# Kernel tuning notes

Measured on AMD Instinct MI355X. Metric: run time of the kernel, lower is better.

Reference implementation:

```python
import math
import jax, jax.numpy as jnp
import numpy as np

C = 1024
H = 16
HD = C // H
T = 2048
B = 2
EPS = 1e-5


def setup_inputs() -> dict:
    key = jax.random.key(0)
    ks = jax.random.split(key, 8)
    s = 0.02
    return {
        "x": jax.random.normal(ks[0], (B, T, C), dtype=jnp.float32),
        "ln1_g": jnp.ones((C,), jnp.float32),
        "ln1_b": jnp.zeros((C,), jnp.float32),
        "w_attn": jax.random.normal(ks[1], (C, 3 * C), dtype=jnp.float32) * s,
        "b_attn": jnp.zeros((3 * C,), jnp.float32),
        "w_proj": jax.random.normal(ks[2], (C, C), dtype=jnp.float32) * s,
        "b_proj": jnp.zeros((C,), jnp.float32),
        "ln2_g": jnp.ones((C,), jnp.float32),
        "ln2_b": jnp.zeros((C,), jnp.float32),
        "w_fc": jax.random.normal(ks[3], (C, 4 * C), dtype=jnp.float32) * s,
        "b_fc": jnp.zeros((4 * C,), jnp.float32),
        "w_fc2": jax.random.normal(ks[4], (4 * C, C), dtype=jnp.float32) * s,
        "b_fc2": jnp.zeros((C,), jnp.float32),
    }


def _layernorm(x, g, b):
    mu = jnp.mean(x, axis=-1, keepdims=True)
    var = jnp.mean((x - mu) ** 2, axis=-1, keepdims=True)
    return (x - mu) * jax.lax.rsqrt(var + EPS) * g + b


def _attention(x, w_attn, b_attn, w_proj, b_proj):
    Bb, Tt, Cc = x.shape
    qkv = x @ w_attn + b_attn  # (B,T,3C)
    q, k, v = jnp.split(qkv, 3, axis=-1)
    # (B,H,T,HD)
    q = q.reshape(Bb, Tt, H, HD).transpose(0, 2, 1, 3)
    k = k.reshape(Bb, Tt, H, HD).transpose(0, 2, 1, 3)
    v = v.reshape(Bb, Tt, H, HD).transpose(0, 2, 1, 3)
    scale = 1.0 / math.sqrt(HD)
    attn = jnp.einsum("bhqd,bhkd->bhqk", q, k) * scale
    causal = jnp.tril(jnp.ones((Tt, Tt), dtype=bool))
    attn = jnp.where(causal[None, None], attn, -jnp.inf)
    attn = jax.nn.softmax(attn, axis=-1)
    out = jnp.einsum("bhqk,bhkd->bhqd", attn, v)
    out = out.transpose(0, 2, 1, 3).reshape(Bb, Tt, Cc)
    return out @ w_proj + b_proj


def _mlp(x, w_fc, b_fc, w_fc2, b_fc2):
    h = jax.nn.gelu(x @ w_fc + b_fc, approximate=True)
    return h @ w_fc2 + b_fc2


def reference(x, ln1_g, ln1_b, w_attn, b_attn, w_proj, b_proj,
              ln2_g, ln2_b, w_fc, b_fc, w_fc2, b_fc2):
    x = x + _attention(_layernorm(x, ln1_g, ln1_b), w_attn, b_attn, w_proj, b_proj)
    x = x + _mlp(_layernorm(x, ln2_g, ln2_b), w_fc, b_fc, w_fc2, b_fc2)
    return x
```

## Files before the change

### kernel.cpp

```cpp
#include <hip/hip_runtime.h>
#include <math.h>

#define TB 2
#define TT 2048
#define TC 1024
#define TH 16
#define THD 64
#define TM (TB*TT)
#define NQT 32

typedef __bf16 bf16x8 __attribute__((ext_vector_type(8)));
typedef float f32x4 __attribute__((ext_vector_type(4)));
typedef unsigned short u16x8 __attribute__((ext_vector_type(8)));
typedef unsigned short u16x4 __attribute__((ext_vector_type(4)));

__device__ __forceinline__ unsigned short f2bf(float f){
    unsigned int u = __builtin_bit_cast(unsigned int, f);
    u = (u + 0x7FFFu + ((u >> 16) & 1u)) >> 16;
    return (unsigned short)u;
}
__device__ __forceinline__ float bf2f(unsigned short h){
    unsigned int u = ((unsigned int)h) << 16;
    return __builtin_bit_cast(float, u);
}
__device__ __forceinline__ bf16x8 ldbf8(const unsigned short* p){
    return __builtin_bit_cast(bf16x8, *(const u16x8*)p);
}
__device__ __forceinline__ void gl_lds16(const void* g, void* l){
    __builtin_amdgcn_global_load_lds(
        (const __attribute__((address_space(1))) unsigned int*)g,
        (__attribute__((address_space(3))) unsigned int*)l,
        16, 0, 0);
}
__device__ __forceinline__ float gelu_tanh(float v){
    float u = 2.0f * 0.7978845608028654f * (v + 0.044715f * v * v * v);
    u = fminf(fmaxf(u, -30.f), 30.f);
    float e = __expf(u);
    return 0.5f * v * (1.f + (e - 1.f) / (e + 1.f));
}

__global__ __launch_bounds__(256)
void convert_all(const float* __restrict__ w_attn, const float* __restrict__ w_proj,
                 const float* __restrict__ w_fc,   const float* __restrict__ w_fc2,
                 unsigned short* __restrict__ wattnT, unsigned short* __restrict__ wprojT,
                 unsigned short* __restrict__ wfcT,   unsigned short* __restrict__ wfc2T){
    __shared__ float tile[32][33];
    const int bid = blockIdx.x;
    const float* in; unsigned short* out; int K, N, bx, by;
    if (bid < 3072)      { in=w_attn; out=wattnT; K=1024; N=3072; bx=bid%96;  by=bid/96; }
    else if (bid < 4096) { int lo=bid-3072; in=w_proj; out=wprojT; K=1024; N=1024; bx=lo%32;  by=lo/32; }
    else if (bid < 8192) { int lo=bid-4096; in=w_fc;   out=wfcT;   K=1024; N=4096; bx=lo%128; by=lo/128; }
    else                 { int lo=bid-8192; in=w_fc2;  out=wfc2T;  K=4096; N=1024; bx=lo%32;  by=lo/32; }
    int tx = threadIdx.x, ty = threadIdx.y;
    int n0 = bx * 32, k0 = by * 32;
    #pragma unroll
    for (int i = 0; i < 4; i++)
        tile[ty + 8*i][tx] = in[(size_t)(k0 + ty + 8*i) * N + n0 + tx];
    __syncthreads();
    #pragma unroll
    for (int i = 0; i < 4; i++)
        out[(size_t)(n0 + ty + 8*i) * K + k0 + tx] = f2bf(tile[tx][ty + 8*i]);
}

__global__ __launch_bounds__(256)
void ln_kernel(const float* __restrict__ x, const float* __restrict__ g,
               const float* __restrict__ be, unsigned short* __restrict__ y){
    const int row = blockIdx.x, t = threadIdx.x;
    const float4* xr = (const float4*)(x + (size_t)row * TC);
    float4 v = xr[t];
    float s  = v.x + v.y + v.z + v.w;
    float s2 = v.x*v.x + v.y*v.y + v.z*v.z + v.w*v.w;
    #pragma unroll
    for (int off = 32; off; off >>= 1){
        s  += __shfl_down(s,  off);
        s2 += __shfl_down(s2, off);
    }
    __shared__ float red[8];
    int l = t & 63, wv = t >> 6;
    if (l == 0){ red[wv] = s; red[4 + wv] = s2; }
    __syncthreads();
    float S  = red[0] + red[1] + red[2] + red[3];
    float S2 = red[4] + red[5] + red[6] + red[7];
    float mu = S * (1.f / TC);
    float var = S2 * (1.f / TC) - mu * mu;
    float rs = rsqrtf(var + 1e-5f);
    int c = t * 4;
    float4 gg = *(const float4*)(g + c);
    float4 bb = *(const float4*)(be + c);
    u16x4 o;
    o[0] = f2bf((v.x - mu) * rs * gg.x + bb.x);
    o[1] = f2bf((v.y - mu) * rs * gg.y + bb.y);
    o[2] = f2bf((v.z - mu) * rs * gg.z + bb.z);
    o[3] = f2bf((v.w - mu) * rs * gg.w + bb.w);
    *(u16x4*)(y + (size_t)row * TC + c) = o;
}

template<int EPI>
__global__ __launch_bounds__(256, 2)
void gemm_bt(const unsigned short* __restrict__ A,
             const unsigned short* __restrict__ Bt,
             const float* __restrict__ bias,
             const float* __restrict__ resid,
             void* __restrict__ outv,
             int M, int N, int K){
    __shared__ unsigned short lA[128 * 32];
    __shared__ unsigned short lB[128 * 32];
    const int t = threadIdx.x, w = t >> 6, l = t & 63, lr = l & 15, lg = l >> 4;
    const int nt = N >> 7;
    const int nwg = gridDim.x;
    const int bid = blockIdx.x;
    int wg = (nwg & 7) ? bid : ((bid & 7) * (nwg >> 3) + (bid >> 3));
    const int bm = wg / nt, bn = wg % nt;
    const int row0 = bm << 7, col0 = bn << 7;
    const int wr = w >> 1, wc = w & 1;

    f32x4 acc[4][4];
    #pragma unroll
    for (int i = 0; i < 4; i++)
        #pragma unroll
        for (int j = 0; j < 4; j++) acc[i][j] = (f32x4){0.f,0.f,0.f,0.f};

    const char* Ag = (const char*)(A + (size_t)(row0 + (t >> 2)) * K) + (t & 3) * 16;
    const char* Bg = (const char*)(Bt + (size_t)(col0 + (t >> 2)) * K) + (t & 3) * 16;
    const size_t rstep = (size_t)64 * K * 2;
    char* lAw = (char*)lA + w * 1024;
    char* lBw = (char*)lB + w * 1024;

    for (int k0 = 0; k0 < K; k0 += 32){
        size_t kb = (size_t)k0 * 2;
        gl_lds16(Ag + kb,          lAw);
        gl_lds16(Ag + kb + rstep,  lAw + 4096);
        gl_lds16(Bg + kb,          lBw);
        gl_lds16(Bg + kb + rstep,  lBw + 4096);
        __syncthreads();
        bf16x8 af[4], bfr[4];
        #pragma unroll
        for (int mi = 0; mi < 4; mi++)
            af[mi] = ldbf8(lA + (wr*64 + mi*16 + lr) * 32 + lg * 8);
        #pragma unroll
        for (int ni = 0; ni < 4; ni++)
            bfr[ni] = ldbf8(lB + (wc*64 + ni*16 + lr) * 32 + lg * 8);
        #pragma unroll
        for (int mi = 0; mi < 4; mi++)
            #pragma unroll
            for (int ni = 0; ni < 4; ni++)
                acc[mi][ni] = __builtin_amdgcn_mfma_f32_16x16x32_bf16(
                    af[mi], bfr[ni], acc[mi][ni], 0, 0, 0);
        __syncthreads();
    }

    float bcol[4];
    #pragma unroll
    for (int ni = 0; ni < 4; ni++) bcol[ni] = bias[col0 + wc*64 + ni*16 + lr];
    #pragma unroll
    for (int mi = 0; mi < 4; mi++){
        #pragma unroll
        for (int j = 0; j < 4; j++){
            int row = row0 + wr*64 + mi*16 + lg*4 + j;
            size_t base = (size_t)row * N + col0 + wc*64 + lr;
            #pragma unroll
            for (int ni = 0; ni < 4; ni++){
                float v = acc[mi][ni][j] + bcol[ni];
                size_t idx = base + (size_t)ni * 16;
                if (EPI == 0)      ((unsigned short*)outv)[idx] = f2bf(v);
                else if (EPI == 1) ((float*)outv)[idx] = v + resid[idx];
                else               ((unsigned short*)outv)[idx] = f2bf(gelu_tanh(v));
            }
        }
    }
}

template<int MH>
__device__ __forceinline__ void gloadA(const unsigned short* bufA, bf16x8 (&af)[4][2],
                                       int wm, int lr, int sl0, int sl1){
    #pragma unroll
    for (int i = 0; i < 4; i++){
        int lrow = (wm*128 + (MH*4 + i)*16 + lr) * 64;
        af[i][0] = ldbf8(bufA + lrow + sl0);
        af[i][1] = ldbf8(bufA + lrow + sl1);
    }
}
__device__ __forceinline__ void gloadB(const unsigned short* bufB, bf16x8 (&bfr)[4][2],
                                       int wn, int lr, int sl0, int sl1){
    #pragma unroll
    for (int i = 0; i < 4; i++){
        int brow = (wn*64 + i*16 + lr) * 64;
        bfr[i][0] = ldbf8(bufB + brow + sl0);
        bfr[i][1] = ldbf8(bufB + brow + sl1);
    }
}
template<int MH, int NH>
__device__ __forceinline__ void gmma(const bf16x8 (&af)[4][2], const bf16x8 (&bfr)[4][2],
                                     f32x4 (&acc)[8][4]){
    #pragma unroll
    for (int i = 0; i < 4; i++)
        #pragma unroll
        for (int j = 0; j < 2; j++){
            f32x4& a = acc[MH*4 + i][NH*2 + j];
            a = __builtin_amdgcn_mfma_f32_16x16x32_bf16(af[i][0], bfr[NH*2+j][0], a, 0,0,0);
            a = __builtin_amdgcn_mfma_f32_16x16x32_bf16(af[i][1], bfr[NH*2+j][1], a, 0,0,0);
        }
}

#define G256_LOOP(NT_, KBEG_)                                                   \
    for (int tk = 0; tk < (NT_); ++tk){                                         \
        const int cur = tk & 1;                                                 \
        const bool more = (tk + 1) < (NT_);                                     \
        const unsigned short* bufA = &lds[cur][0][0];                           \
        const unsigned short* bufB = &lds[cur][1][0];                           \
        if (more){                                                              \
            stage(cur ^ 1, (KBEG_) + (tk + 1)*64, 0);                           \
            asm volatile("s_waitcnt vmcnt(2)" ::: "memory");                    \
        } else {                                                                \
            asm volatile("s_waitcnt vmcnt(0)" ::: "memory");                    \
        }                                                                       \
        __builtin_amdgcn_s_barrier();                                           \
        bf16x8 af[4][2], bfr[4][2];                                             \
        gloadA<0>(bufA, af, wm, lr, sl0, sl1);                                  \
        gloadB(bufB, bfr, wn, lr, sl0, sl1);                                    \
        if (more) stage(cur ^ 1, (KBEG_) + (tk + 1)*64, 1);                     \
        __builtin_amdgcn_s_barrier();                                           \
        asm volatile("s_waitcnt lgkmcnt(0)" ::: "memory");                      \
        __builtin_amdgcn_sched_barrier(0);                                      \
        __builtin_amdgcn_s_setprio(1);                                          \
        gmma<0,0>(af, bfr, acc);                                                \
        __builtin_amdgcn_s_setprio(0);                                          \
        __builtin_amdgcn_s_barrier();                                           \
        if (more) stage(cur ^ 1, (KBEG_) + (tk + 1)*64, 2);                     \
        __builtin_amdgcn_s_setprio(1);                                          \
        gmma<0,1>(af, bfr, acc);                                                \
        __builtin_amdgcn_s_setprio(0);                                          \
        __builtin_amdgcn_s_barrier();                                           \
        gloadA<1>(bufA, af, wm, lr, sl0, sl1);                                  \
        if (more) stage(cur ^ 1, (KBEG_) + (tk + 1)*64, 3);                     \
        __builtin_amdgcn_s_barrier();                                           \
        asm volatile("s_waitcnt lgkmcnt(0)" ::: "memory");                      \
        __builtin_amdgcn_sched_barrier(0);                                      \
        __builtin_amdgcn_s_setprio(1);                                          \
        gmma<1,0>(af, bfr, acc);                                                \
        __builtin_amdgcn_s_setprio(0);                                          \
        __builtin_amdgcn_s_barrier();                                           \
        __builtin_amdgcn_s_setprio(1);                                          \
        gmma<1,1>(af, bfr, acc);                                                \
        __builtin_amdgcn_s_setprio(0);                                          \
        __builtin_amdgcn_s_barrier();                                           \
    }

template<int EPI>
__global__ __launch_bounds__(512, 1)
void gemm256(const unsigned short* __restrict__ A,
             const unsigned short* __restrict__ Bt,
             const float* __restrict__ bias,
             void* __restrict__ outv,
             int M, int N, int K){
    __shared__ unsigned short lds[2][2][256*64];
    const int t = threadIdx.x;
    const int w = t >> 6, l = t & 63, lr = l & 15, lg = l >> 4;
    const int wm = w >> 2, wn = w & 3;
    const int lr7 = lr & 7;
    const int sl0 = (lg ^ lr7) << 3;
    const int sl1 = ((4 + lg) ^ lr7) << 3;
    const int nbn = N >> 8;
    const int nwg = (M >> 8) * nbn;
    const int bid = blockIdx.x;
    const int wg = (nwg & 7) ? bid : ((bid & 7) * (nwg >> 3) + (bid >> 3));
    const int bm = wg / nbn, bn = wg % nbn;
    const size_t row0 = (size_t)bm << 8, col0 = (size_t)bn << 8;
    const int NT = K >> 6;

    f32x4 acc[8][4];
    #pragma unroll
    for (int i = 0; i < 8; i++)
        #pragma unroll
        for (int j = 0; j < 4; j++) acc[i][j] = (f32x4){0.f,0.f,0.f,0.f};

    int rowc[4], slogc[4];
    #pragma unroll
    for (int c = 0; c < 4; c++){
        int seg = t + (c << 9);
        rowc[c]  = seg >> 3;
        slogc[c] = (((seg & 7) ^ ((seg >> 3) & 7)) << 3);
    }
    const unsigned short* Abase = A  + row0 * K;
    const unsigned short* Bbase = Bt + col0 * K;
    auto stage = [&](int buf, int kofs, int c){
        int seg = t + (c << 9);
        const unsigned short* sa = Abase + (size_t)rowc[c] * K + kofs + slogc[c];
        const unsigned short* sb = Bbase + (size_t)rowc[c] * K + kofs + slogc[c];
        gl_lds16(sa, (void*)&lds[buf][0][seg * 8]);
        gl_lds16(sb, (void*)&lds[buf][1][seg * 8]);
    };

    #pragma unroll
    for (int c = 0; c < 4; c++) stage(0, 0, c);

    G256_LOOP(NT, 0)

    float bcol[4];
    #pragma unroll
    for (int ni = 0; ni < 4; ni++) bcol[ni] = bias[col0 + wn*64 + ni*16 + lr];
    unsigned short* outp = (unsigned short*)outv;
    #pragma unroll
    for (int mi = 0; mi < 8; mi++){
        #pragma unroll
        for (int j = 0; j < 4; j++){
            size_t row = row0 + wm*128 + mi*16 + lg*4 + j;
            size_t base = row * N + col0 + wn*64 + lr;
            #pragma unroll
            for (int ni = 0; ni < 4; ni++){
                float v = acc[mi][ni][j] + bcol[ni];
                size_t idx = base + (size_t)ni * 16;
                if (EPI == 0) outp[idx] = f2bf(v);
                else          outp[idx] = f2bf(gelu_tanh(v));
            }
        }
    }
}

__global__ __launch_bounds__(512, 1)
void gemm256sk(const unsigned short* __restrict__ A,
               const unsigned short* __restrict__ Bt,
               unsigned short* __restrict__ pout,
               int M, int N, int K, int klen){
    __shared__ unsigned short lds[2][2][256*64];
    const int t = threadIdx.x;
    const int w = t >> 6, l = t & 63, lr = l & 15, lg = l >> 4;
    const int wm = w >> 2, wn = w & 3;
    const int lr7 = lr & 7;
    const int sl0 = (lg ^ lr7) << 3;
    const int sl1 = ((4 + lg) ^ lr7) << 3;
    const int nbn = N >> 8;
    const int ntile = (M >> 8) * nbn;
    const int nwg = gridDim.x;
    const int bid = blockIdx.x;
    int wg = (nwg & 7) ? bid : ((bid & 7) * (nwg >> 3) + (bid >> 3));
    const int kh = wg / ntile;
    wg -= kh * ntile;
    const int bm = wg / nbn, bn = wg % nbn;
    const size_t row0 = (size_t)bm << 8, col0 = (size_t)bn << 8;
    const int NT = klen >> 6;
    const int kbeg = kh * klen;

    f32x4 acc[8][4];
    #pragma unroll
    for (int i = 0; i < 8; i++)
        #pragma unroll
        for (int j = 0; j < 4; j++) acc[i][j] = (f32x4){0.f,0.f,0.f,0.f};

    int rowc[4], slogc[4];
    #pragma unroll
    for (int c = 0; c < 4; c++){
        int seg = t + (c << 9);
        rowc[c]  = seg >> 3;
        slogc[c] = (((seg & 7) ^ ((seg >> 3) & 7)) << 3);
    }
    const unsigned short* Abase = A  + row0 * K;
    const unsigned short* Bbase = Bt + col0 * K;
    auto stage = [&](int buf, int kofs, int c){
        int seg = t + (c << 9);
        const unsigned short* sa = Abase + (size_t)rowc[c] * K + kofs + slogc[c];
        const unsigned short* sb = Bbase + (size_t)rowc[c] * K + kofs + slogc[c];
        gl_lds16(sa, (void*)&lds[buf][0][seg * 8]);
        gl_lds16(sb, (void*)&lds[buf][1][seg * 8]);
    };

    #pragma unroll
    for (int c = 0; c < 4; c++) stage(0, kbeg, c);

    G256_LOOP(NT, kbeg)

    unsigned short* outp = pout + (size_t)kh * M * N;
    #pragma unroll
    for (int mi = 0; mi < 8; mi++){
        #pragma unroll
        for (int j = 0; j < 4; j++){
            size_t row = row0 + wm*128 + mi*16 + lg*4 + j;
            size_t base = row * N + col0 + wn*64 + lr;
            #pragma unroll
            for (int ni = 0; ni < 4; ni++)
                outp[base + (size_t)ni * 16] = f2bf(acc[mi][ni][j]);
        }
    }
}

__global__ __launch_bounds__(256)
void combine_k4(const unsigned short* __restrict__ p,
                const float* __restrict__ bias, const float* __restrict__ resid,
                float* __restrict__ out){
    const size_t PS = (size_t)TM * TC;
    const int total = TM * TC / 4;
    for (int i = blockIdx.x * 256 + threadIdx.x; i < total; i += gridDim.x * 256){
        int e = i * 4;
        u16x4 a0 = *(const u16x4*)(p + e);
        u16x4 a1 = *(const u16x4*)(p + PS + e);
        u16x4 a2 = *(const u16x4*)(p + 2*PS + e);
        u16x4 a3 = *(const u16x4*)(p + 3*PS + e);
        float4 r = *(const float4*)(resid + e);
        float4 bb = *(const float4*)(bias + (e & (TC - 1)));
        float4 o;
        o.x = bf2f(a0[0]) + bf2f(a1[0]) + bf2f(a2[0]) + bf2f(a3[0]) + r.x + bb.x;
        o.y = bf2f(a0[1]) + bf2f(a1[1]) + bf2f(a2[1]) + bf2f(a3[1]) + r.y + bb.y;
        o.z = bf2f(a0[2]) + bf2f(a1[2]) + bf2f(a2[2]) + bf2f(a3[2]) + r.z + bb.z;
        o.w = bf2f(a0[3]) + bf2f(a1[3]) + bf2f(a2[3]) + bf2f(a3[3]) + r.w + bb.w;
        *(float4*)(out + e) = o;
    }
}

__global__ __launch_bounds__(256)
void vtrans(const unsigned short* __restrict__ qkv, unsigned short* __restrict__ vTg){
    __shared__ unsigned short lt[64][68];
    int kt = blockIdx.x & (NQT - 1);
    int bh = blockIdx.x >> 5;
    int h = bh & (TH - 1), b = bh >> 4;
    int t = threadIdx.x;
    int r = t >> 2, c4 = t & 3;
    const unsigned short* src = qkv + (size_t)(b*TT + kt*64 + r) * (3*TC) + 2*TC + h*THD;
    u16x8 a0 = *(const u16x8*)(src + c4*8);
    u16x8 a1 = *(const u16x8*)(src + 32 + c4*8);
    #pragma unroll
    for (int j = 0; j < 8; j++){
        lt[r][c4*8 + j]      = a0[j];
        lt[r][32 + c4*8 + j] = a1[j];
    }
    __syncthreads();
    int d = t >> 2;
    unsigned short* dst = vTg + ((size_t)bh * NQT + kt) * (64*80) + (size_t)d * 80;
    u16x8 o0, o1;
    #pragma unroll
    for (int j = 0; j < 8; j++){
        o0[j] = lt[c4*8 + j][d];
        o1[j] = lt[32 + c4*8 + j][d];
    }
    *(u16x8*)(dst + c4*8)      = o0;
    *(u16x8*)(dst + 32 + c4*8) = o1;
}

__global__ __launch_bounds__(256, 3)
void attn_kernel(const unsigned short* __restrict__ qkv,
                 const unsigned short* __restrict__ vTg,
                 unsigned short* __restrict__ attn_out){
    __shared__ unsigned short kbuf[2][64*64];
    __shared__ unsigned short vbuf[2][64*64];
    __shared__ unsigned short pl[4][16*72];

    const int bid = blockIdx.x;
    const int qrank = bid >> 5;
    const int bh = bid & 31;
    const int h = bh & (TH - 1), b = bh >> 4;
    const int qb = 31 - qrank;
    const int q0 = qb << 6;
    const int t = threadIdx.x, w = t >> 6, l = t & 63, lr = l & 15, lg = l >> 4;
    const int lr7 = lr & 7;
    const int sl0 = (lg ^ lr7) << 3;
    const int sl1 = ((4 + lg) ^ lr7) << 3;
    const float SC = 0.18033688011112042f;

    const int NKT = qb + 1;
    const int qrow_base = q0 + w*16;

    const int vt0 = t, vt1 = t + 256;
    const int sr0 = vt0 >> 3, sr1 = vt1 >> 3;
    const int sc0 = ((vt0 & 7) ^ (sr0 & 7)) * 8;
    const int sc1 = ((vt1 & 7) ^ (sr1 & 7)) * 8;
    const unsigned short* kg0 = qkv + (size_t)(b*TT + sr0) * (3*TC) + TC + h*THD + sc0;
    const unsigned short* kg1 = qkv + (size_t)(b*TT + sr1) * (3*TC) + TC + h*THD + sc1;
    const unsigned short* vg0 = vTg + (size_t)bh * (NQT*64*80) + (size_t)sr0 * 80 + sc0;
    const unsigned short* vg1 = vTg + (size_t)bh * (NQT*64*80) + (size_t)sr1 * 80 + sc1;
    const size_t kstep = (size_t)64 * (3*TC);

    auto stage = [&](int kt, int buf){
        gl_lds16(kg0 + (size_t)kt*kstep,   (void*)&kbuf[buf][vt0*8]);
        gl_lds16(kg1 + (size_t)kt*kstep,   (void*)&kbuf[buf][vt1*8]);
        gl_lds16(vg0 + (size_t)kt*(64*80), (void*)&vbuf[buf][vt0*8]);
        gl_lds16(vg1 + (size_t)kt*(64*80), (void*)&vbuf[buf][vt1*8]);
    };

    const unsigned short* qr =
        qkv + (size_t)(b*TT + qrow_base + lr) * (3*TC) + h*THD;
    bf16x8 q0f = ldbf8(qr + lg*8), q1f = ldbf8(qr + 32 + lg*8);

    bf16x8 ones;
    #pragma unroll
    for (int i = 0; i < 8; i++) ones[i] = (__bf16)1.0f;

    f32x4 o[5];
    float m[4];
    #pragma unroll
    for (int i = 0; i < 5; i++) o[i] = (f32x4){0.f,0.f,0.f,0.f};
    #pragma unroll
    for (int i = 0; i < 4; i++) m[i] = -1e30f;

    unsigned short* plw = &pl[w][0];

    stage(0, 0);
    for (int kt = 0; kt < NKT; ++kt){
        const int cur = kt & 1;
        const bool more = (kt + 1) < NKT;
        if (more){
            stage(kt + 1, cur ^ 1);
            asm volatile("s_waitcnt vmcnt(4)" ::: "memory");
        } else {
            asm volatile("s_waitcnt vmcnt(0)" ::: "memory");
        }
        __builtin_amdgcn_s_barrier();

        const unsigned short* kb = &kbuf[cur][0];
        f32x4 s[4];
        __builtin_amdgcn_s_setprio(1);
        #pragma unroll
        for (int cb = 0; cb < 4; cb++){
            bf16x8 ka = ldbf8(kb + (cb*16 + lr)*64 + sl0);
            bf16x8 kbf = ldbf8(kb + (cb*16 + lr)*64 + sl1);
            f32x4 z = (f32x4){0.f,0.f,0.f,0.f};
            z = __builtin_amdgcn_mfma_f32_16x16x32_bf16(q0f, ka, z, 0,0,0);
            z = __builtin_amdgcn_mfma_f32_16x16x32_bf16(q1f, kbf, z, 0,0,0);
            s[cb] = z;
        }
        __builtin_amdgcn_s_setprio(0);
        if (kt == qb){
            #pragma unroll
            for (int cb = 0; cb < 4; cb++)
                #pragma unroll
                for (int j = 0; j < 4; j++)
                    if (kt*64 + cb*16 + lr > qrow_base + lg*4 + j) s[cb][j] = -1e30f;
        }
        float mloc[4];
        #pragma unroll
        for (int j = 0; j < 4; j++)
            mloc[j] = fmaxf(fmaxf(s[0][j], s[1][j]), fmaxf(s[2][j], s[3][j]));
        #pragma unroll
        for (int off = 1; off < 16; off <<= 1)
            #pragma unroll
            for (int j = 0; j < 4; j++)
                mloc[j] = fmaxf(mloc[j], __shfl_xor(mloc[j], off));
        bool grow = (mloc[0]*SC > m[0]) || (mloc[1]*SC > m[1]) ||
                    (mloc[2]*SC > m[2]) || (mloc[3]*SC > m[3]);
        if (__any(grow)){
            float al[4];
            #pragma unroll
            for (int j = 0; j < 4; j++){
                float mn = fmaxf(m[j], mloc[j] * SC);
                al[j] = exp2f(m[j] - mn);
                m[j] = mn;
            }
            #pragma unroll
            for (int db = 0; db < 5; db++)
                #pragma unroll
                for (int j = 0; j < 4; j++) o[db][j] *= al[j];
        }
        #pragma unroll
        for (int cb = 0; cb < 4; cb++)
            #pragma unroll
            for (int j = 0; j < 4; j++){
                float e = exp2f(__builtin_fmaf(s[cb][j], SC, -m[j]));
                ((__bf16*)plw)[(lg*4 + j)*72 + cb*16 + lr] = (__bf16)e;
            }
        const unsigned short* vb = &vbuf[cur][0];
        bf16x8 pa0 = ldbf8(plw + lr*72 + lg*8);
        bf16x8 pa1 = ldbf8(plw + lr*72 + 32 + lg*8);
        __builtin_amdgcn_s_setprio(1);
        #pragma unroll
        for (int db = 0; db < 4; db++){
            bf16x8 va = ldbf8(vb + (db*16 + lr)*64 + sl0);
            bf16x8 vbf = ldbf8(vb + (db*16 + lr)*64 + sl1);
            o[db] = __builtin_amdgcn_mfma_f32_16x16x32_bf16(pa0, va, o[db], 0,0,0);
            o[db] = __builtin_amdgcn_mfma_f32_16x16x32_bf16(pa1, vbf, o[db], 0,0,0);
        }
        o[4] = __builtin_amdgcn_mfma_f32_16x16x32_bf16(pa0, ones, o[4], 0,0,0);
        o[4] = __builtin_amdgcn_mfma_f32_16x16x32_bf16(pa1, ones, o[4], 0,0,0);
        __builtin_amdgcn_s_setprio(0);

        __builtin_amdgcn_s_barrier();
    }

    __bf16* aout = (__bf16*)attn_out;
    #pragma unroll
    for (int j = 0; j < 4; j++){
        float inv = 1.f / o[4][j];
        size_t tok = (size_t)(b*TT + qrow_base + lg*4 + j);
        #pragma unroll
        for (int db = 0; db < 4; db++)
            aout[tok*TC + h*THD + db*16 + lr] = (__bf16)(o[db][j] * inv);
    }
}

extern "C" void kernel_launch(void* const* d_in, const int* in_sizes, int n_in,
                              void* d_out, int out_size, void* d_ws, size_t ws_size,
                              hipStream_t stream){
    const float* x      = (const float*)d_in[0];
    const float* ln1_g  = (const float*)d_in[1];
    const float* ln1_b  = (const float*)d_in[2];
    const float* w_attn = (const float*)d_in[3];
    const float* b_attn = (const float*)d_in[4];
    const float* w_proj = (const float*)d_in[5];
    const float* b_proj = (const float*)d_in[6];
    const float* ln2_g  = (const float*)d_in[7];
    const float* ln2_b  = (const float*)d_in[8];
    const float* w_fc   = (const float*)d_in[9];
    const float* b_fc   = (const float*)d_in[10];
    const float* w_fc2  = (const float*)d_in[11];
    const float* b_fc2  = (const float*)d_in[12];
    float* out = (float*)d_out;

    char* ws = (char*)d_ws;
    size_t off = 0;
    auto alloc = [&](size_t bytes) -> void* {
        void* p = ws + off;
        off += (bytes + 255) & ~(size_t)255;
        return p;
    };
    unsigned short* wattnT = (unsigned short*)alloc((size_t)3072*1024*2);
    unsigned short* wprojT = (unsigned short*)alloc((size_t)1024*1024*2);
    unsigned short* wfcT   = (unsigned short*)alloc((size_t)4096*1024*2);
    unsigned short* wfc2T  = (unsigned short*)alloc((size_t)1024*4096*2);
    unsigned short* xn1    = (unsigned short*)alloc((size_t)TM*TC*2);
    unsigned short* qkvb   = (unsigned short*)alloc((size_t)TM*3*TC*2);
    float*          resid1 = (float*)alloc((size_t)TM*TC*4);
    unsigned short* xn2    = (unsigned short*)alloc((size_t)TM*TC*2);
    unsigned short* hbuf   = (unsigned short*)alloc((size_t)TM*4*TC*2);
    unsigned short* attnO  = (unsigned short*)alloc((size_t)TM*TC*2);
    unsigned short* vTg    = (unsigned short*)alloc((size_t)TB*TH*NQT*64*80*2);

    unsigned short* pks = xn1;

    convert_all<<<12288, dim3(32, 8, 1), 0, stream>>>(
        w_attn, w_proj, w_fc, w_fc2, wattnT, wprojT, wfcT, wfc2T);

    ln_kernel<<<TM, 256, 0, stream>>>(x, ln1_g, ln1_b, xn1);

    gemm256<0><<<(TM/256)*(3072/256), 512, 0, stream>>>(
        xn1, wattnT, b_attn, qkvb, TM, 3072, 1024);

    vtrans<<<TB*TH*NQT, 256, 0, stream>>>(qkvb, vTg);

    attn_kernel<<<TB*TH*NQT, 256, 0, stream>>>(qkvb, vTg, attnO);

    gemm_bt<1><<<(TM/128)*(1024/128), 256, 0, stream>>>(
        attnO, wprojT, b_proj, x, resid1, TM, 1024, 1024);

    ln_kernel<<<TM, 256, 0, stream>>>(resid1, ln2_g, ln2_b, xn2);

    gemm256<2><<<(TM/256)*(4096/256), 512, 0, stream>>>(
        xn2, wfcT, b_fc, hbuf, TM, 4096, 1024);

    gemm256sk<<<4*(TM/256)*(1024/256), 512, 0, stream>>>(
        hbuf, wfc2T, pks, TM, 1024, 4096, 1024);
    combine_k4<<<2048, 256, 0, stream>>>(pks, b_fc2, resid1, out);
}
```

Measured before the change: 237.3 us.

## Fuse LN1 into weight-prep launch and single-buffer attention K/V for occupancy

The first layernorm is folded into the weight-conversion kernel as extra blocks, which removes one kernel launch and lets the two independent jobs run side by side. The attention kernel drops double-buffered K/V shared memory for a single buffer and raises the launch-bounds occupancy hint from 3 to 4 blocks. Each next tile is now loaded only after the trailing barrier, so the load no longer overlaps compute within a block. The design relies on the extra resident blocks to hide that latency instead.

```diff
diff --git a/kernel.cpp b/kernel.cpp
--- a/kernel.cpp
+++ b/kernel.cpp
@@ -40,18 +40,52 @@
 }
 
 __global__ __launch_bounds__(256)
-void convert_all(const float* __restrict__ w_attn, const float* __restrict__ w_proj,
-                 const float* __restrict__ w_fc,   const float* __restrict__ w_fc2,
-                 unsigned short* __restrict__ wattnT, unsigned short* __restrict__ wprojT,
-                 unsigned short* __restrict__ wfcT,   unsigned short* __restrict__ wfc2T){
+void prep_all(const float* __restrict__ w_attn, const float* __restrict__ w_proj,
+              const float* __restrict__ w_fc,   const float* __restrict__ w_fc2,
+              unsigned short* __restrict__ wattnT, unsigned short* __restrict__ wprojT,
+              unsigned short* __restrict__ wfcT,   unsigned short* __restrict__ wfc2T,
+              const float* __restrict__ x, const float* __restrict__ ln1_g,
+              const float* __restrict__ ln1_b, unsigned short* __restrict__ xn1){
+    const int bid = blockIdx.x;
+    const int t = threadIdx.x;
+    if (bid >= 12288){
+        const int row = bid - 12288;
+        const float4* xr = (const float4*)(x + (size_t)row * TC);
+        float4 v = xr[t];
+        float s  = v.x + v.y + v.z + v.w;
+        float s2 = v.x*v.x + v.y*v.y + v.z*v.z + v.w*v.w;
+        #pragma unroll
+        for (int off = 32; off; off >>= 1){
+            s  += __shfl_down(s,  off);
+            s2 += __shfl_down(s2, off);
+        }
+        __shared__ float red[8];
+        int l = t & 63, wv = t >> 6;
+        if (l == 0){ red[wv] = s; red[4 + wv] = s2; }
+        __syncthreads();
+        float S  = red[0] + red[1] + red[2] + red[3];
+        float S2 = red[4] + red[5] + red[6] + red[7];
+        float mu = S * (1.f / TC);
+        float var = S2 * (1.f / TC) - mu * mu;
+        float rs = rsqrtf(var + 1e-5f);
+        int c = t * 4;
+        float4 gg = *(const float4*)(ln1_g + c);
+        float4 bb = *(const float4*)(ln1_b + c);
+        u16x4 o;
+        o[0] = f2bf((v.x - mu) * rs * gg.x + bb.x);
+        o[1] = f2bf((v.y - mu) * rs * gg.y + bb.y);
+        o[2] = f2bf((v.z - mu) * rs * gg.z + bb.z);
+        o[3] = f2bf((v.w - mu) * rs * gg.w + bb.w);
+        *(u16x4*)(xn1 + (size_t)row * TC + c) = o;
+        return;
+    }
     __shared__ float tile[32][33];
-    const int bid = blockIdx.x;
     const float* in; unsigned short* out; int K, N, bx, by;
     if (bid < 3072)      { in=w_attn; out=wattnT; K=1024; N=3072; bx=bid%96;  by=bid/96; }
     else if (bid < 4096) { int lo=bid-3072; in=w_proj; out=wprojT; K=1024; N=1024; bx=lo%32;  by=lo/32; }
     else if (bid < 8192) { int lo=bid-4096; in=w_fc;   out=wfcT;   K=1024; N=4096; bx=lo%128; by=lo/128; }
     else                 { int lo=bid-8192; in=w_fc2;  out=wfc2T;  K=4096; N=1024; bx=lo%32;  by=lo/32; }
-    int tx = threadIdx.x, ty = threadIdx.y;
+    int tx = t & 31, ty = t >> 5;
     int n0 = bx * 32, k0 = by * 32;
     #pragma unroll
     for (int i = 0; i < 4; i++)
@@ -435,12 +469,12 @@
     *(u16x8*)(dst + 32 + c4*8) = o1;
 }
 
-__global__ __launch_bounds__(256, 3)
+__global__ __launch_bounds__(256, 4)
 void attn_kernel(const unsigned short* __restrict__ qkv,
                  const unsigned short* __restrict__ vTg,
                  unsigned short* __restrict__ attn_out){
-    __shared__ unsigned short kbuf[2][64*64];
-    __shared__ unsigned short vbuf[2][64*64];
+    __shared__ unsigned short kbuf[64*64];
+    __shared__ unsigned short vbuf[64*64];
     __shared__ unsigned short pl[4][16*72];
 
     const int bid = blockIdx.x;
@@ -468,11 +502,11 @@
     const unsigned short* vg1 = vTg + (size_t)bh * (NQT*64*80) + (size_t)sr1 * 80 + sc1;
     const size_t kstep = (size_t)64 * (3*TC);
 
-    auto stage = [&](int kt, int buf){
-        gl_lds16(kg0 + (size_t)kt*kstep,   (void*)&kbuf[buf][vt0*8]);
-        gl_lds16(kg1 + (size_t)kt*kstep,   (void*)&kbuf[buf][vt1*8]);
-        gl_lds16(vg0 + (size_t)kt*(64*80), (void*)&vbuf[buf][vt0*8]);
-        gl_lds16(vg1 + (size_t)kt*(64*80), (void*)&vbuf[buf][vt1*8]);
+    auto stage = [&](int kt){
+        gl_lds16(kg0 + (size_t)kt*kstep,   (void*)&kbuf[vt0*8]);
+        gl_lds16(kg1 + (size_t)kt*kstep,   (void*)&kbuf[vt1*8]);
+        gl_lds16(vg0 + (size_t)kt*(64*80), (void*)&vbuf[vt0*8]);
+        gl_lds16(vg1 + (size_t)kt*(64*80), (void*)&vbuf[vt1*8]);
     };
 
     const unsigned short* qr =
@@ -492,25 +526,17 @@
 
     unsigned short* plw = &pl[w][0];
 
-    stage(0, 0);
+    stage(0);
     for (int kt = 0; kt < NKT; ++kt){
-        const int cur = kt & 1;
-        const bool more = (kt + 1) < NKT;
-        if (more){
-            stage(kt + 1, cur ^ 1);
-            asm volatile("s_waitcnt vmcnt(4)" ::: "memory");
-        } else {
-            asm volatile("s_waitcnt vmcnt(0)" ::: "memory");
-        }
+        asm volatile("s_waitcnt vmcnt(0)" ::: "memory");
         __builtin_amdgcn_s_barrier();
 
-        const unsigned short* kb = &kbuf[cur][0];
         f32x4 s[4];
         __builtin_amdgcn_s_setprio(1);
         #pragma unroll
         for (int cb = 0; cb < 4; cb++){
-            bf16x8 ka = ldbf8(kb + (cb*16 + lr)*64 + sl0);
-            bf16x8 kbf = ldbf8(kb + (cb*16 + lr)*64 + sl1);
+            bf16x8 ka = ldbf8(kbuf + (cb*16 + lr)*64 + sl0);
+            bf16x8 kbf = ldbf8(kbuf + (cb*16 + lr)*64 + sl1);
             f32x4 z = (f32x4){0.f,0.f,0.f,0.f};
             z = __builtin_amdgcn_mfma_f32_16x16x32_bf16(q0f, ka, z, 0,0,0);
             z = __builtin_amdgcn_mfma_f32_16x16x32_bf16(q1f, kbf, z, 0,0,0);
@@ -555,14 +581,13 @@
                 float e = exp2f(__builtin_fmaf(s[cb][j], SC, -m[j]));
                 ((__bf16*)plw)[(lg*4 + j)*72 + cb*16 + lr] = (__bf16)e;
             }
-        const unsigned short* vb = &vbuf[cur][0];
         bf16x8 pa0 = ldbf8(plw + lr*72 + lg*8);
         bf16x8 pa1 = ldbf8(plw + lr*72 + 32 + lg*8);
         __builtin_amdgcn_s_setprio(1);
         #pragma unroll
         for (int db = 0; db < 4; db++){
-            bf16x8 va = ldbf8(vb + (db*16 + lr)*64 + sl0);
-            bf16x8 vbf = ldbf8(vb + (db*16 + lr)*64 + sl1);
+            bf16x8 va = ldbf8(vbuf + (db*16 + lr)*64 + sl0);
+            bf16x8 vbf = ldbf8(vbuf + (db*16 + lr)*64 + sl1);
             o[db] = __builtin_amdgcn_mfma_f32_16x16x32_bf16(pa0, va, o[db], 0,0,0);
             o[db] = __builtin_amdgcn_mfma_f32_16x16x32_bf16(pa1, vbf, o[db], 0,0,0);
         }
@@ -571,6 +596,7 @@
         __builtin_amdgcn_s_setprio(0);
 
         __builtin_amdgcn_s_barrier();
+        if (kt + 1 < NKT) stage(kt + 1);
     }
 
     __bf16* aout = (__bf16*)attn_out;
@@ -623,10 +649,9 @@
 
     unsigned short* pks = xn1;
 
-    convert_all<<<12288, dim3(32, 8, 1), 0, stream>>>(
-        w_attn, w_proj, w_fc, w_fc2, wattnT, wprojT, wfcT, wfc2T);
-
-    ln_kernel<<<TM, 256, 0, stream>>>(x, ln1_g, ln1_b, xn1);
+    prep_all<<<12288 + TM, 256, 0, stream>>>(
+        w_attn, w_proj, w_fc, w_fc2, wattnT, wprojT, wfcT, wfc2T,
+        x, ln1_g, ln1_b, xn1);
 
     gemm256<0><<<(TM/256)*(3072/256), 512, 0, stream>>>(
         xn1, wattnT, b_attn, qkvb, TM, 3072, 1024);
```

Result: no change. 235.2 us (-0.9%).
